# Optimization experiments

Hardware: AMD Instinct MI355X
Metric: run time of the kernel (lower is better)

## Reference

```python
import jax, jax.numpy as jnp
import numpy as np

INPUT_DIM = 512
N_CLASSES = 100
N_SUBNETS = 20
HIDDEN = 32
WS1 = INPUT_DIM * HIDDEN   # 16384
BS1 = HIDDEN               # 32
WS2 = HIDDEN * N_CLASSES   # 3200
BS2 = N_CLASSES            # 100
TOTAL = WS1 + BS1 + WS2 + BS2  # 19716
LN_EPS = 1e-5


def _layernorm(v, g, b):
    mu = jnp.mean(v, axis=-1, keepdims=True)
    var = jnp.mean(jnp.square(v - mu), axis=-1, keepdims=True)
    return (v - mu) * jax.lax.rsqrt(var + LN_EPS) * g + b


def setup_inputs() -> dict:
    key = jax.random.key(0)
    ks = jax.random.split(key, 12)
    def lin(k, fan_in, shape):
        bound = 1.0 / np.sqrt(fan_in)
        return jax.random.uniform(k, shape, jnp.float32, -bound, bound)
    return {
        "x": jax.random.normal(ks[0], (32768, INPUT_DIM), jnp.float32),
        "W_h1": lin(ks[1], INPUT_DIM, (128, INPUT_DIM)),
        "b_h1": lin(ks[2], INPUT_DIM, (128,)),
        "g1": jnp.ones((128,), jnp.float32),
        "be1": jnp.zeros((128,), jnp.float32),
        "W_h2": lin(ks[3], 128, (256, 128)),
        "b_h2": lin(ks[4], 128, (256,)),
        "g2": jnp.ones((256,), jnp.float32),
        "be2": jnp.zeros((256,), jnp.float32),
        "W_h3": lin(ks[5], 256, (N_SUBNETS * TOTAL, 256)),
        "b_h3": lin(ks[6], 256, (N_SUBNETS * TOTAL,)),
        "ens_w": jnp.full((N_SUBNETS,), 1.0 / N_SUBNETS, jnp.float32),
    }


def reference(x, W_h1, b_h1, g1, be1, W_h2, b_h2, g2, be2, W_h3, b_h3, ens_w):
    # context from support set (= x itself): (1, input_dim)
    context = jnp.mean(x, axis=0, keepdims=True)
    # hypernet MLP (eval mode: dropout = identity)
    h = jax.nn.relu(_layernorm(context @ W_h1.T + b_h1, g1, be1))
    h = jax.nn.relu(_layernorm(h @ W_h2.T + b_h2, g2, be2))
    all_params = (h @ W_h3.T + b_h3).reshape(N_SUBNETS, TOTAL)
    # split generated params (same layout as torch .view)
    W1 = all_params[:, :WS1].reshape(N_SUBNETS, HIDDEN, INPUT_DIM)       # (S,H,I)
    b1 = all_params[:, WS1:WS1 + BS1]                                     # (S,H)
    W2 = all_params[:, WS1 + BS1:WS1 + BS1 + WS2].reshape(N_SUBNETS, N_CLASSES, HIDDEN)  # (S,C,H)
    b2 = all_params[:, WS1 + BS1 + WS2:]                                  # (S,C)
    # batched per-subnet 2-layer nets (dropout p=0.2 is identity in eval)
    hh = jax.nn.relu(jnp.einsum('bi,shi->sbh', x, W1) + b1[:, None, :])   # (S,B,H)
    logits = jnp.einsum('sbh,sch->sbc', hh, W2) + b2[:, None, :]          # (S,B,C)
    w = jax.nn.softmax(ens_w)                                             # (S,)
    return jnp.einsum('s,sbc->bc', w, logits)                             # (B,C)
```

## Files before the change

### kernel.cpp

```cpp
#include <hip/hip_runtime.h>
#include <hip/hip_bf16.h>

#define BATCH   32768
#define DIM     512
#define H1N     128
#define H2N     256
#define NSUB    20
#define HID     32
#define NCLS    100
#define NHID    640
#define TOTALP  19716
#define NPAR    394320
#define WS1P    16384
#define WS1B1   16416
#define WS2END  19616

#define OFF_PART 0
#define OFF_H    262144
#define OFF_W    262400
#define OFF_B1   262432
#define OFF_B2R  263072
#define OFF_W1B  265072
#define OFF_W2B  428912
#define OFF_XB   469872

typedef __attribute__((ext_vector_type(8))) short short8;
typedef __attribute__((ext_vector_type(4))) float f32x4;

static __device__ inline unsigned short f2bf(float f) {
    __hip_bfloat16 h = __float2bfloat16(f);
    return *reinterpret_cast<unsigned short*>(&h);
}

static __device__ __forceinline__ void gload16(const void* g, void* l) {
    __builtin_amdgcn_global_load_lds(
        (const __attribute__((address_space(1))) void*)g,
        (__attribute__((address_space(3))) void*)l, 16, 0, 0);
}

__global__ __launch_bounds__(256) void k1_colsum(const float* __restrict__ x,
                                                 float* __restrict__ F) {
    __shared__ float sP[DIM];
    int t = threadIdx.x, bid = blockIdx.x;
    int par = t >> 7;
    int c4 = (t & 127) * 4;
    const float* xb = x + (size_t)bid * 64 * DIM;
    unsigned short* ob = (unsigned short*)(F + OFF_XB) + (size_t)bid * 64 * DIM;
    float4 acc = make_float4(0.f, 0.f, 0.f, 0.f);
    #pragma unroll 8
    for (int i = 0; i < 32; ++i) {
        int r = 2 * i + par;
        float4 v = *(const float4*)(xb + r * DIM + c4);
        acc.x += v.x; acc.y += v.y; acc.z += v.z; acc.w += v.w;
        ushort4 u;
        u.x = f2bf(v.x); u.y = f2bf(v.y); u.z = f2bf(v.z); u.w = f2bf(v.w);
        *(ushort4*)(ob + r * DIM + c4) = u;
    }
    if (par == 0) *(float4*)(sP + c4) = acc;
    __syncthreads();
    if (par == 1) {
        float4 p = *(const float4*)(sP + c4);
        p.x += acc.x; p.y += acc.y; p.z += acc.z; p.w += acc.w;
        *(float4*)(F + OFF_PART + bid * DIM + c4) = p;
    }
}

__global__ __launch_bounds__(256) void k2_hyper(
    const float* __restrict__ Wh1, const float* __restrict__ bh1,
    const float* __restrict__ g1,  const float* __restrict__ be1,
    const float* __restrict__ Wh2, const float* __restrict__ bh2,
    const float* __restrict__ g2,  const float* __restrict__ be2,
    const float* __restrict__ ensw, float* __restrict__ F)
{
    __shared__ __align__(16) float sctx[DIM];
    __shared__ __align__(16) float sP2[DIM];
    __shared__ __align__(16) float sh1[H1N];
    __shared__ __align__(16) float sh2[H2N];
    int t = threadIdx.x;

    {
        int c4 = (t & 127) * 4;
        int half = t >> 7;
        float4 a = make_float4(0.f, 0.f, 0.f, 0.f);
        #pragma unroll 8
        for (int b = half * 256; b < half * 256 + 256; ++b) {
            float4 v = *(const float4*)(F + OFF_PART + b * DIM + c4);
            a.x += v.x; a.y += v.y; a.z += v.z; a.w += v.w;
        }
        if (half == 0) *(float4*)(sP2 + c4) = a;
        __syncthreads();
        if (half == 1) {
            float4 o = *(const float4*)(sP2 + c4);
            o.x = (o.x + a.x) * (1.0f / BATCH);
            o.y = (o.y + a.y) * (1.0f / BATCH);
            o.z = (o.z + a.z) * (1.0f / BATCH);
            o.w = (o.w + a.w) * (1.0f / BATCH);
            *(float4*)(sctx + c4) = o;
        }
        __syncthreads();
    }

    if (t < H1N) {
        float v = bh1[t];
        const float4* w = (const float4*)(Wh1 + t * DIM);
        for (int k = 0; k < DIM / 4; ++k) {
            float4 ww = w[k]; float4 c = *(const float4*)(sctx + k * 4);
            v += ww.x * c.x + ww.y * c.y + ww.z * c.z + ww.w * c.w;
        }
        sh1[t] = v;
    }
    __syncthreads();
    {
        float mu = 0.f;
        for (int k = 0; k < H1N; ++k) mu += sh1[k];
        mu *= (1.0f / H1N);
        float var = 0.f;
        for (int k = 0; k < H1N; ++k) { float d = sh1[k] - mu; var += d * d; }
        var *= (1.0f / H1N);
        float inv = rsqrtf(var + 1e-5f);
        __syncthreads();
        if (t < H1N) {
            float v = (sh1[t] - mu) * inv * g1[t] + be1[t];
            sh1[t] = fmaxf(v, 0.f);
        }
        __syncthreads();
    }

    {
        float v = bh2[t];
        const float4* w = (const float4*)(Wh2 + t * H1N);
        for (int k = 0; k < H1N / 4; ++k) {
            float4 ww = w[k]; float4 c = *(const float4*)(sh1 + k * 4);
            v += ww.x * c.x + ww.y * c.y + ww.z * c.z + ww.w * c.w;
        }
        sh2[t] = v;
    }
    __syncthreads();
    {
        float mu = 0.f;
        for (int k = 0; k < H2N; ++k) mu += sh2[k];
        mu *= (1.0f / H2N);
        float var = 0.f;
        for (int k = 0; k < H2N; ++k) { float d = sh2[k] - mu; var += d * d; }
        var *= (1.0f / H2N);
        float inv = rsqrtf(var + 1e-5f);
        float v = (sh2[t] - mu) * inv * g2[t] + be2[t];
        F[OFF_H + t] = fmaxf(v, 0.f);
    }

    if (t == 0) {
        float m = -1e30f;
        for (int s = 0; s < NSUB; ++s) m = fmaxf(m, ensw[s]);
        float sum = 0.f, e[NSUB];
        for (int s = 0; s < NSUB; ++s) { e[s] = __expf(ensw[s] - m); sum += e[s]; }
        for (int s = 0; s < NSUB; ++s) F[OFF_W + s] = e[s] / sum;
    }
}

static __device__ __forceinline__ void k3_pack(float* F, int row, float val) {
    __hip_bfloat16* W1B = (__hip_bfloat16*)(F + OFF_W1B);
    __hip_bfloat16* W2B = (__hip_bfloat16*)(F + OFF_W2B);
    int s = row / TOTALP;
    int r = row - s * TOTALP;
    if (r < WS1P) {
        int hh = r >> 9, k = r & 511;
        W1B[(s * HID + hh) * DIM + k] = __float2bfloat16(val);
    } else if (r < WS1B1) {
        F[OFF_B1 + s * HID + (r - WS1P)] = val;
    } else if (r < WS2END) {
        int q = r - WS1B1; int c = q >> 5, hh = q & 31;
        float ws = F[OFF_W + s];
        W2B[c * NHID + s * HID + hh] = __float2bfloat16(ws * val);
    } else {
        F[OFF_B2R + s * NCLS + (r - WS2END)] = val;
    }
}

__global__ __launch_bounds__(256) void k3_gemv(
    const float* __restrict__ Wh3, const float* __restrict__ bh3, float* __restrict__ F)
{
    int t = threadIdx.x;
    int wid = t >> 6, lane = t & 63;
    int row0 = blockIdx.x * 8 + wid * 2;
    const float4 h = *(const float4*)(F + OFF_H + lane * 4);
    const float4 w0 = *(const float4*)(Wh3 + (size_t)row0 * 256 + lane * 4);
    const float4 w1 = *(const float4*)(Wh3 + (size_t)(row0 + 1) * 256 + lane * 4);
    float d0 = w0.x * h.x + w0.y * h.y + w0.z * h.z + w0.w * h.w;
    float d1 = w1.x * h.x + w1.y * h.y + w1.z * h.z + w1.w * h.w;
    #pragma unroll
    for (int off = 32; off; off >>= 1) {
        d0 += __shfl_down(d0, off);
        d1 += __shfl_down(d1, off);
    }
    if (lane == 0) {
        k3_pack(F, row0,     d0 + bh3[row0]);
        k3_pack(F, row0 + 1, d1 + bh3[row0 + 1]);
    }
}

__global__ __launch_bounds__(256) void gemm_fused(
    const __hip_bfloat16* __restrict__ XB, const __hip_bfloat16* __restrict__ W1B,
    const __hip_bfloat16* __restrict__ W2B, const float* __restrict__ F,
    float* __restrict__ out)
{
    __shared__ __align__(16) unsigned char sA[2][64 * 128];
    __shared__ __align__(16) unsigned char sB[2][128 * 128];
    __shared__ __align__(16) unsigned char sP[64 * 256];
    const int t = threadIdx.x;
    int bid = blockIdx.x;
    const int cpx = gridDim.x >> 3;
    bid = (bid & 7) * cpx + (bid >> 3);
    const int Row0 = bid * 64;
    const int wid = t >> 6, lane = t & 63;
    const int l16 = lane & 15, lq = lane >> 4;

    f32x4 acc1[8], acc2[8];
    #pragma unroll
    for (int fn = 0; fn < 8; ++fn) acc2[fn] = (f32x4){0.f, 0.f, 0.f, 0.f};

    auto stage1 = [&](int n1, int kc, int b) {
        #pragma unroll
        for (int i = 0; i < 2; ++i) {
            int cidx = wid * 2 + i;
            int ul = cidx * 64 + lane;
            int row = ul >> 3, u = ul & 7;
            gload16(XB + (size_t)(Row0 + row) * 512 + kc + ((u ^ (row & 7)) << 3),
                    &sA[b][cidx * 1024]);
        }
        #pragma unroll
        for (int i = 0; i < 4; ++i) {
            int cidx = wid * 4 + i;
            int ul = cidx * 64 + lane;
            int row = ul >> 3, u = ul & 7;
            gload16(W1B + (size_t)(n1 * 128 + row) * 512 + kc + ((u ^ (row & 7)) << 3),
                    &sB[b][cidx * 1024]);
        }
    };
    auto stageW2 = [&](int n1, int h, int b) {
        #pragma unroll
        for (int i = 0; i < 4; ++i) {
            int cidx = wid * 4 + i;
            int ul = cidx * 64 + lane;
            int row = ul >> 3, u = ul & 7;
            gload16(W2B + (size_t)row * NHID + n1 * 128 + h * 64 + ((u ^ (row & 7)) << 3),
                    &sB[b][cidx * 1024]);
        }
    };
    auto comp1 = [&](int b) {
        #pragma unroll
        for (int kk = 0; kk < 2; ++kk) {
            int u = kk * 4 + lq;
            int arow = wid * 16 + l16;
            short8 af = *(const short8*)(&sA[b][arow * 128 + ((u ^ (arow & 7)) << 4)]);
            short8 bfv[8];
            #pragma unroll
            for (int fn = 0; fn < 8; ++fn) {
                int rw = fn * 16 + l16;
                bfv[fn] = *(const short8*)(&sB[b][rw * 128 + ((u ^ (rw & 7)) << 4)]);
            }
            #pragma unroll
            for (int fn = 0; fn < 8; ++fn)
                acc1[fn] = __builtin_amdgcn_mfma_f32_16x16x32_bf16(
                    af, bfv[fn], acc1[fn], 0, 0, 0);
        }
    };
    auto comp2 = [&](int h, int b) {
        #pragma unroll
        for (int kk = 0; kk < 2; ++kk) {
            int u = kk * 4 + lq;
            int punit = (h * 2 + kk) * 4 + lq;
            int arow = wid * 16 + l16;
            short8 af = *(const short8*)(&sP[arow * 256 + ((punit ^ (arow & 7)) << 4)]);
            short8 bfv[8];
            #pragma unroll
            for (int fn = 0; fn < 8; ++fn) {
                int rw = fn * 16 + l16;
                bfv[fn] = *(const short8*)(&sB[b][rw * 128 + ((u ^ (rw & 7)) << 4)]);
            }
            #pragma unroll
            for (int fn = 0; fn < 8; ++fn)
                acc2[fn] = __builtin_amdgcn_mfma_f32_16x16x32_bf16(
                    af, bfv[fn], acc2[fn], 0, 0, 0);
        }
    };

    int buf = 0;
    stage1(0, 0, 0);
    float b1r[8];

    for (int n1 = 0; n1 < 5; ++n1) {
        #pragma unroll
        for (int st = 0; st < 10; ++st) {
            if (st < 9) {
                if (st + 1 < 8) stage1(n1, (st + 1) * 64, buf ^ 1);
                else stageW2(n1, st + 1 - 8, buf ^ 1);
            } else if (n1 < 4) {
                stage1(n1 + 1, 0, buf ^ 1);
            }
            if (st < 9) {
                if (st + 1 < 8) asm volatile("s_waitcnt vmcnt(6)" ::: "memory");
                else            asm volatile("s_waitcnt vmcnt(4)" ::: "memory");
            } else if (n1 < 4) {
                asm volatile("s_waitcnt vmcnt(6)" ::: "memory");
            } else {
                asm volatile("s_waitcnt vmcnt(0)" ::: "memory");
            }
            __builtin_amdgcn_s_barrier();
            __builtin_amdgcn_sched_barrier(0);

            if (st == 0) {
                #pragma unroll
                for (int fn = 0; fn < 8; ++fn) {
                    acc1[fn] = (f32x4){0.f, 0.f, 0.f, 0.f};
                    b1r[fn] = F[OFF_B1 + n1 * 128 + fn * 16 + l16];
                }
            }
            if (st < 8) comp1(buf);
            else comp2(st - 8, buf);
            if (st == 7) {
                #pragma unroll
                for (int fn = 0; fn < 8; ++fn) {
                    int col = fn * 16 + l16;
                    int unit = col >> 3;
                    #pragma unroll
                    for (int r = 0; r < 4; ++r) {
                        int row = wid * 16 + lq * 4 + r;
                        float v = fmaxf(acc1[fn][r] + b1r[fn], 0.f);
                        *(unsigned short*)(&sP[row * 256 + ((unit ^ (row & 7)) << 4)
                                           + (col & 7) * 2]) = f2bf(v);
                    }
                }
            }
            __builtin_amdgcn_sched_barrier(0);
            __builtin_amdgcn_s_barrier();
            buf ^= 1;
        }
    }

    float* sBe = (float*)&sA[0][0];
    if (t < 128) {
        float b = 0.f;
        if (t < NCLS) {
            #pragma unroll
            for (int s = 0; s < NSUB; ++s)
                b += F[OFF_W + s] * F[OFF_B2R + s * NCLS + t];
        }
        sBe[t] = b;
    }
    __syncthreads();

    #pragma unroll
    for (int fn = 0; fn < 8; ++fn) {
        int gcol = fn * 16 + l16;
        if (gcol < NCLS) {
            float be = sBe[gcol];
            #pragma unroll
            for (int r = 0; r < 4; ++r) {
                int grow = Row0 + wid * 16 + lq * 4 + r;
                out[(size_t)grow * NCLS + gcol] = acc2[fn][r] + be;
            }
        }
    }
}

extern "C" void kernel_launch(void* const* d_in, const int* in_sizes, int n_in,
                              void* d_out, int out_size, void* d_ws, size_t ws_size,
                              hipStream_t stream)
{
    const float* x    = (const float*)d_in[0];
    const float* Wh1  = (const float*)d_in[1];
    const float* bh1  = (const float*)d_in[2];
    const float* g1   = (const float*)d_in[3];
    const float* be1  = (const float*)d_in[4];
    const float* Wh2  = (const float*)d_in[5];
    const float* bh2  = (const float*)d_in[6];
    const float* g2   = (const float*)d_in[7];
    const float* be2  = (const float*)d_in[8];
    const float* Wh3  = (const float*)d_in[9];
    const float* bh3  = (const float*)d_in[10];
    const float* ensw = (const float*)d_in[11];
    float* F = (float*)d_ws;
    float* out = (float*)d_out;

    const __hip_bfloat16* XB  = (const __hip_bfloat16*)(F + OFF_XB);
    const __hip_bfloat16* W1B = (const __hip_bfloat16*)(F + OFF_W1B);
    const __hip_bfloat16* W2B = (const __hip_bfloat16*)(F + OFF_W2B);

    k1_colsum<<<512, 256, 0, stream>>>(x, F);
    k2_hyper<<<1, 256, 0, stream>>>(Wh1, bh1, g1, be1, Wh2, bh2, g2, be2, ensw, F);
    k3_gemv<<<NPAR / 8, 256, 0, stream>>>(Wh3, bh3, F);
    gemm_fused<<<BATCH / 64, 256, 0, stream>>>(XB, W1B, W2B, F, out);
}
```

Measured before the change: 192.6 us.

## Load x rows directly into register A-fragments, drop bf16 x staging buffer

The colsum kernel no longer writes a bf16 copy of x to workspace. The fused GEMM instead loads each wave's 16 fp32 rows of x once, converts them to bf16, and keeps all 16 K-fragments in registers for reuse across the 5 N-chunks. This removes the 32MB bf16 write and its re-reads, and the per-step LDS staging of A. In exchange it adds 64 VGPRs for the fragments, which may lower occupancy, and x is now read twice (colsum and GEMM).

```diff
diff --git a/kernel.cpp b/kernel.cpp
--- a/kernel.cpp
+++ b/kernel.cpp
@@ -22,7 +22,6 @@
 #define OFF_B2R  263072
 #define OFF_W1B  265072
 #define OFF_W2B  428912
-#define OFF_XB   469872
 
 typedef __attribute__((ext_vector_type(8))) short short8;
 typedef __attribute__((ext_vector_type(4))) float f32x4;
@@ -45,16 +44,12 @@
     int par = t >> 7;
     int c4 = (t & 127) * 4;
     const float* xb = x + (size_t)bid * 64 * DIM;
-    unsigned short* ob = (unsigned short*)(F + OFF_XB) + (size_t)bid * 64 * DIM;
     float4 acc = make_float4(0.f, 0.f, 0.f, 0.f);
     #pragma unroll 8
     for (int i = 0; i < 32; ++i) {
         int r = 2 * i + par;
         float4 v = *(const float4*)(xb + r * DIM + c4);
         acc.x += v.x; acc.y += v.y; acc.z += v.z; acc.w += v.w;
-        ushort4 u;
-        u.x = f2bf(v.x); u.y = f2bf(v.y); u.z = f2bf(v.z); u.w = f2bf(v.w);
-        *(ushort4*)(ob + r * DIM + c4) = u;
     }
     if (par == 0) *(float4*)(sP + c4) = acc;
     __syncthreads();
@@ -199,11 +194,10 @@
 }
 
 __global__ __launch_bounds__(256) void gemm_fused(
-    const __hip_bfloat16* __restrict__ XB, const __hip_bfloat16* __restrict__ W1B,
+    const float* __restrict__ x, const __hip_bfloat16* __restrict__ W1B,
     const __hip_bfloat16* __restrict__ W2B, const float* __restrict__ F,
     float* __restrict__ out)
 {
-    __shared__ __align__(16) unsigned char sA[2][64 * 128];
     __shared__ __align__(16) unsigned char sB[2][128 * 128];
     __shared__ __align__(16) unsigned char sP[64 * 256];
     const int t = threadIdx.x;
@@ -218,15 +212,7 @@
     #pragma unroll
     for (int fn = 0; fn < 8; ++fn) acc2[fn] = (f32x4){0.f, 0.f, 0.f, 0.f};
 
-    auto stage1 = [&](int n1, int kc, int b) {
-        #pragma unroll
-        for (int i = 0; i < 2; ++i) {
-            int cidx = wid * 2 + i;
-            int ul = cidx * 64 + lane;
-            int row = ul >> 3, u = ul & 7;
-            gload16(XB + (size_t)(Row0 + row) * 512 + kc + ((u ^ (row & 7)) << 3),
-                    &sA[b][cidx * 1024]);
-        }
+    auto stageW1 = [&](int n1, int kc, int b) {
         #pragma unroll
         for (int i = 0; i < 4; ++i) {
             int cidx = wid * 4 + i;
@@ -246,12 +232,33 @@
                     &sB[b][cidx * 1024]);
         }
     };
-    auto comp1 = [&](int b) {
+
+    stageW1(0, 0, 0);
+
+    short8 afr[16];
+    {
+        const float* xrow = x + (size_t)(Row0 + wid * 16 + l16) * 512;
+        #pragma unroll
+        for (int i = 0; i < 16; ++i) {
+            int k0 = (i >> 1) * 64 + (i & 1) * 32 + lq * 8;
+            float4 a = *(const float4*)(xrow + k0);
+            float4 b = *(const float4*)(xrow + k0 + 4);
+            unsigned int p[4];
+            p[0] = (unsigned)f2bf(a.x) | ((unsigned)f2bf(a.y) << 16);
+            p[1] = (unsigned)f2bf(a.z) | ((unsigned)f2bf(a.w) << 16);
+            p[2] = (unsigned)f2bf(b.x) | ((unsigned)f2bf(b.y) << 16);
+            p[3] = (unsigned)f2bf(b.z) | ((unsigned)f2bf(b.w) << 16);
+            afr[i] = *(short8*)p;
+        }
+    }
+    asm volatile("s_waitcnt vmcnt(0)" ::: "memory");
+    __builtin_amdgcn_s_barrier();
+
+    auto comp1 = [&](int st, int b) {
         #pragma unroll
         for (int kk = 0; kk < 2; ++kk) {
             int u = kk * 4 + lq;
-            int arow = wid * 16 + l16;
-            short8 af = *(const short8*)(&sA[b][arow * 128 + ((u ^ (arow & 7)) << 4)]);
+            short8 af = afr[st * 2 + kk];
             short8 bfv[8];
             #pragma unroll
             for (int fn = 0; fn < 8; ++fn) {
@@ -285,26 +292,20 @@
     };
 
     int buf = 0;
-    stage1(0, 0, 0);
     float b1r[8];
-
     for (int n1 = 0; n1 < 5; ++n1) {
         #pragma unroll
         for (int st = 0; st < 10; ++st) {
             if (st < 9) {
-                if (st + 1 < 8) stage1(n1, (st + 1) * 64, buf ^ 1);
+                if (st + 1 < 8) stageW1(n1, (st + 1) * 64, buf ^ 1);
                 else stageW2(n1, st + 1 - 8, buf ^ 1);
             } else if (n1 < 4) {
-                stage1(n1 + 1, 0, buf ^ 1);
-            }
-            if (st < 9) {
-                if (st + 1 < 8) asm volatile("s_waitcnt vmcnt(6)" ::: "memory");
-                else            asm volatile("s_waitcnt vmcnt(4)" ::: "memory");
-            } else if (n1 < 4) {
-                asm volatile("s_waitcnt vmcnt(6)" ::: "memory");
-            } else {
+                stageW1(n1 + 1, 0, buf ^ 1);
+            }
+            if (st == 9 && n1 == 4)
                 asm volatile("s_waitcnt vmcnt(0)" ::: "memory");
-            }
+            else
+                asm volatile("s_waitcnt vmcnt(4)" ::: "memory");
             __builtin_amdgcn_s_barrier();
             __builtin_amdgcn_sched_barrier(0);
 
@@ -315,7 +316,7 @@
                     b1r[fn] = F[OFF_B1 + n1 * 128 + fn * 16 + l16];
                 }
             }
-            if (st < 8) comp1(buf);
+            if (st < 8) comp1(st, buf);
             else comp2(st - 8, buf);
             if (st == 7) {
                 #pragma unroll
@@ -337,7 +338,7 @@
         }
     }
 
-    float* sBe = (float*)&sA[0][0];
+    float* sBe = (float*)sP;
     if (t < 128) {
         float b = 0.f;
         if (t < NCLS) {
@@ -382,12 +383,11 @@
     float* F = (float*)d_ws;
     float* out = (float*)d_out;
 
-    const __hip_bfloat16* XB  = (const __hip_bfloat16*)(F + OFF_XB);
     const __hip_bfloat16* W1B = (const __hip_bfloat16*)(F + OFF_W1B);
     const __hip_bfloat16* W2B = (const __hip_bfloat16*)(F + OFF_W2B);
 
     k1_colsum<<<512, 256, 0, stream>>>(x, F);
     k2_hyper<<<1, 256, 0, stream>>>(Wh1, bh1, g1, be1, Wh2, bh2, g2, be2, ensw, F);
     k3_gemv<<<NPAR / 8, 256, 0, stream>>>(Wh3, bh3, F);
-    gemm_fused<<<BATCH / 64, 256, 0, stream>>>(XB, W1B, W2B, F, out);
-}
+    gemm_fused<<<BATCH / 64, 256, 0, stream>>>(x, W1B, W2B, F, out);
+}
```

After: 182.9 us. 1.05x faster.
